# Optimization experiments

Measured on AMD Instinct MI355X. Metric: run time of the kernel, lower is better.

The kernel has to match this reference:

```python
import jax, jax.numpy as jnp
import numpy as np

EPS = 1e-5

def _ln(x):
    # non-affine LayerNorm over last dim
    m = jnp.mean(x, axis=-1, keepdims=True)
    v = jnp.var(x, axis=-1, keepdims=True)
    return (x - m) / jnp.sqrt(v + EPS)

def setup_inputs() -> dict:
    key = jax.random.key(0)
    ks = jax.random.split(key, 6)
    B, D_in, H = 16384, 512, 512
    bound_i = 1.0 / np.sqrt(D_in)
    bound_h = 1.0 / np.sqrt(H)
    x = jax.random.normal(ks[0], (B, D_in), dtype=jnp.float32)
    hx = jax.random.normal(ks[1], (B, H), dtype=jnp.float32)
    W_i2h = jax.random.uniform(ks[2], (3 * H, D_in), minval=-bound_i, maxval=bound_i, dtype=jnp.float32)
    b_i2h = jax.random.uniform(ks[3], (3 * H,), minval=-bound_i, maxval=bound_i, dtype=jnp.float32)
    W_h2h = jax.random.uniform(ks[4], (3 * H, H), minval=-bound_h, maxval=bound_h, dtype=jnp.float32)
    b_h2h = jax.random.uniform(ks[5], (3 * H,), minval=-bound_h, maxval=bound_h, dtype=jnp.float32)
    return {"x": x, "hx": hx, "W_i2h": W_i2h, "b_i2h": b_i2h, "W_h2h": W_h2h, "b_h2h": b_h2h}

def reference(x, hx, W_i2h, b_i2h, W_h2h, b_h2h):
    H = hx.shape[-1]
    xt = x @ W_i2h.T + b_i2h        # [B, 3H]
    ht = hx @ W_h2h.T + b_h2h       # [B, 3H]
    x_new = xt[:, 2 * H:]
    h_new = ht[:, 2 * H:]
    gates = jax.nn.sigmoid(_ln(xt[:, : 2 * H]) + _ln(ht[:, : 2 * H]))
    r_t = gates[:, :H]
    z_t = gates[:, H:]
    n_t = jnp.tanh(_ln(x_new) + r_t * _ln(h_new))
    h_t = z_t * hx + (1.0 - z_t) * n_t
    return h_t
```

## Files before the change

kernel.cpp:

```cpp
#include <hip/hip_runtime.h>

#define M_ROWS 16384
#define N_COLS 1536
#define K_DIM  512
#define H_DIM  512

typedef __attribute__((ext_vector_type(8))) short short8;
typedef __attribute__((ext_vector_type(16))) float f32x16;

__device__ __forceinline__ unsigned short f2bf(float f) {
  unsigned u = __float_as_uint(f);
  u += 0x7fffu + ((u >> 16) & 1u);
  return (unsigned short)(u >> 16);
}
__device__ __forceinline__ float bf2f(unsigned short h) {
  return __uint_as_float(((unsigned)h) << 16);
}

__device__ __forceinline__ void gload_lds16(const void* g, void* l) {
  __builtin_amdgcn_global_load_lds((const __attribute__((address_space(1))) void*)g,
                                   (__attribute__((address_space(3))) void*)l,
                                   16, 0, 0);
}

__global__ __launch_bounds__(256) void cvt_all(
    const float* __restrict__ x, const float* __restrict__ hx,
    const float* __restrict__ Wi, const float* __restrict__ Wh,
    unsigned short* __restrict__ xb, unsigned short* __restrict__ hxb,
    unsigned short* __restrict__ Wib, unsigned short* __restrict__ Whb) {
  int i = blockIdx.x * blockDim.x + threadIdx.x;
  const float* s; unsigned short* d; int off;
  if (i < 2097152)      { s = x;  d = xb;  off = i; }
  else if (i < 4194304) { s = hx; d = hxb; off = i - 2097152; }
  else if (i < 4390912) { s = Wi; d = Wib; off = i - 4194304; }
  else                  { s = Wh; d = Whb; off = i - 4390912; }
  float4 f = ((const float4*)s)[off];
  ushort4 u;
  u.x = f2bf(f.x); u.y = f2bf(f.y); u.z = f2bf(f.z); u.w = f2bf(f.w);
  ((ushort4*)d)[off] = u;
}

__global__ __launch_bounds__(256, 4) void gemm_bf16(
    const unsigned short* __restrict__ xb, const unsigned short* __restrict__ hxb,
    const unsigned short* __restrict__ Wib, const unsigned short* __restrict__ Whb,
    const float* __restrict__ b_i2h, const float* __restrict__ b_h2h,
    unsigned short* __restrict__ xt, unsigned short* __restrict__ ht) {
  const int mat = blockIdx.z;
  const unsigned short* A  = mat ? hxb : xb;
  const unsigned short* Bw = mat ? Whb : Wib;
  const float* bias        = mat ? b_h2h : b_i2h;
  unsigned short* outp     = mat ? ht : xt;

  const int m0 = blockIdx.x * 128;
  const int n0 = blockIdx.y * 128;

  __shared__ short lds[2 * 128 * 64];
  short* ldsA = lds;
  short* ldsB = lds + 128 * 64;

  const int t = threadIdx.x;
  const int w = t >> 6, lane = t & 63;
  const int w_row = w >> 1, w_col = w & 1;
  const int l31 = lane & 31, h = lane >> 5;

  f32x16 acc[2][2];
#pragma unroll
  for (int i = 0; i < 2; ++i)
#pragma unroll
    for (int j = 0; j < 2; ++j)
#pragma unroll
      for (int r = 0; r < 16; ++r) acc[i][j][r] = 0.f;

  const int srow = lane >> 3;
  const int scol = ((lane & 7) ^ srow) * 8;

  for (int k0 = 0; k0 < K_DIM; k0 += 64) {
#pragma unroll
    for (int q = 0; q < 4; ++q) {
      const int base_row = w * 32 + q * 8;
      gload_lds16(A  + (size_t)(m0 + base_row + srow) * K_DIM + k0 + scol,
                  &ldsA[base_row * 64]);
      gload_lds16(Bw + (size_t)(n0 + base_row + srow) * K_DIM + k0 + scol,
                  &ldsB[base_row * 64]);
    }
    __syncthreads();
#pragma unroll
    for (int kk = 0; kk < 4; ++kk) {
      const int chunk = ((kk * 2 + h) ^ (l31 & 7)) * 8;
      short8 af[2], bf[2];
#pragma unroll
      for (int i = 0; i < 2; ++i)
        af[i] = *(const short8*)&ldsA[(w_row * 64 + i * 32 + l31) * 64 + chunk];
#pragma unroll
      for (int j = 0; j < 2; ++j)
        bf[j] = *(const short8*)&ldsB[(w_col * 64 + j * 32 + l31) * 64 + chunk];
#pragma unroll
      for (int i = 0; i < 2; ++i)
#pragma unroll
        for (int j = 0; j < 2; ++j)
          acc[i][j] = __builtin_amdgcn_mfma_f32_32x32x16_bf16(af[i], bf[j], acc[i][j], 0, 0, 0);
    }
    __syncthreads();
  }

  float bj0[2], bj1[2];
#pragma unroll
  for (int j = 0; j < 2; ++j) {
    bj0[j] = bias[n0 + w_col * 64 + 0 * 32 + l31] * 0.f;
  }
  const float biasj0 = bias[n0 + w_col * 64 + l31];
  const float biasj1 = bias[n0 + w_col * 64 + 32 + l31];

#pragma unroll
  for (int i = 0; i < 2; ++i) {
#pragma unroll
    for (int g = 0; g < 4; ++g) {
#pragma unroll
      for (int d = 0; d < 4; ++d) {
        const int reg = g * 4 + d;
        const int row = d + 8 * g + 4 * h;
        ushort2 pk;
        pk.x = f2bf(acc[i][0][reg] + biasj0);
        pk.y = f2bf(acc[i][1][reg] + biasj1);
        *(ushort2*)(outp + (size_t)(m0 + w_row * 64 + i * 32 + row) * N_COLS +
                    n0 + w_col * 64 + 2 * l31) = pk;
      }
    }
  }
}

__global__ __launch_bounds__(256) void finalize_kernel(
    const unsigned short* __restrict__ xt, const unsigned short* __restrict__ ht,
    const unsigned short* __restrict__ hxb, float* __restrict__ out) {
  const int w = threadIdx.x >> 6, lane = threadIdx.x & 63;
  const int b = blockIdx.x * 4 + w;
  const size_t rb = (size_t)b * N_COLS;

  short8 sxr = *(const short8*)&xt[rb + 8 * lane];
  short8 sxz = *(const short8*)&xt[rb + 512 + 8 * lane];
  short8 sxn = *(const short8*)&xt[rb + 1024 + 8 * lane];
  short8 shr = *(const short8*)&ht[rb + 8 * lane];
  short8 shz = *(const short8*)&ht[rb + 512 + 8 * lane];
  short8 shn = *(const short8*)&ht[rb + 1024 + 8 * lane];

  float vxr[8], vxz[8], vxn[8], vhr[8], vhz[8], vhn[8];
#pragma unroll
  for (int k = 0; k < 8; ++k) {
    vxr[k] = bf2f((unsigned short)sxr[k]);
    vxz[k] = bf2f((unsigned short)sxz[k]);
    vxn[k] = bf2f((unsigned short)sxn[k]);
    vhr[k] = bf2f((unsigned short)shr[k]);
    vhz[k] = bf2f((unsigned short)shz[k]);
    vhn[k] = bf2f((unsigned short)shn[k]);
  }

  float pr[8] = {0.f, 0.f, 0.f, 0.f, 0.f, 0.f, 0.f, 0.f};
#pragma unroll
  for (int k = 0; k < 8; ++k) {
    pr[0] += vxr[k] + vxz[k];
    pr[1] += vxr[k] * vxr[k] + vxz[k] * vxz[k];
    pr[2] += vxn[k];
    pr[3] += vxn[k] * vxn[k];
    pr[4] += vhr[k] + vhz[k];
    pr[5] += vhr[k] * vhr[k] + vhz[k] * vhz[k];
    pr[6] += vhn[k];
    pr[7] += vhn[k] * vhn[k];
  }
#pragma unroll
  for (int msk = 1; msk < 64; msk <<= 1)
#pragma unroll
    for (int k = 0; k < 8; ++k) pr[k] += __shfl_xor(pr[k], msk);

  const float inv2H = 1.f / 1024.f, invH = 1.f / 512.f;
  const float mx0 = pr[0] * inv2H;
  const float ix0 = rsqrtf(pr[1] * inv2H - mx0 * mx0 + 1e-5f);
  const float mx1 = pr[2] * invH;
  const float ix1 = rsqrtf(pr[3] * invH - mx1 * mx1 + 1e-5f);
  const float mh0 = pr[4] * inv2H;
  const float ih0 = rsqrtf(pr[5] * inv2H - mh0 * mh0 + 1e-5f);
  const float mh1 = pr[6] * invH;
  const float ih1 = rsqrtf(pr[7] * invH - mh1 * mh1 + 1e-5f);

  auto calc = [&](float xrv, float xzv, float xnv, float hrv, float hzv,
                  float hnv, float hxs) -> float {
    float ar = (xrv - mx0) * ix0 + (hrv - mh0) * ih0;
    float az = (xzv - mx0) * ix0 + (hzv - mh0) * ih0;
    float r = 1.f / (1.f + __expf(-ar));
    float z = 1.f / (1.f + __expf(-az));
    float arg = (xnv - mx1) * ix1 + r * ((hnv - mh1) * ih1);
    float e2 = __expf(2.f * arg);
    float nn = (e2 - 1.f) / (e2 + 1.f);
    return z * hxs + (1.f - z) * nn;
  };

  const int base4 = 64 * (lane >> 3) + 4 * (lane & 7);
  const unsigned short* hxrow = hxb + (size_t)b * H_DIM;
  float* orow = out + (size_t)b * H_DIM;

  ushort4 hx0u = *(const ushort4*)&hxrow[base4];
  ushort4 hx1u = *(const ushort4*)&hxrow[base4 + 32];
  float hx0[4] = {bf2f(hx0u.x), bf2f(hx0u.y), bf2f(hx0u.z), bf2f(hx0u.w)};
  float hx1[4] = {bf2f(hx1u.x), bf2f(hx1u.y), bf2f(hx1u.z), bf2f(hx1u.w)};

  float4 r0, r1;
  float* r0p = (float*)&r0;
  float* r1p = (float*)&r1;
#pragma unroll
  for (int k = 0; k < 4; ++k) {
    r0p[k] = calc(vxr[2 * k], vxz[2 * k], vxn[2 * k],
                  vhr[2 * k], vhz[2 * k], vhn[2 * k], hx0[k]);
    r1p[k] = calc(vxr[2 * k + 1], vxz[2 * k + 1], vxn[2 * k + 1],
                  vhr[2 * k + 1], vhz[2 * k + 1], vhn[2 * k + 1], hx1[k]);
  }
  *(float4*)&orow[base4] = r0;
  *(float4*)&orow[base4 + 32] = r1;
}

extern "C" void kernel_launch(void* const* d_in, const int* in_sizes, int n_in,
                              void* d_out, int out_size, void* d_ws, size_t ws_size,
                              hipStream_t stream) {
  const float* x  = (const float*)d_in[0];
  const float* hx = (const float*)d_in[1];
  const float* Wi = (const float*)d_in[2];
  const float* bi = (const float*)d_in[3];
  const float* Wh = (const float*)d_in[4];
  const float* bh = (const float*)d_in[5];
  float* out = (float*)d_out;

  char* ws = (char*)d_ws;
  unsigned short* xb  = (unsigned short*)(ws);
  unsigned short* hxb = (unsigned short*)(ws + 16777216);
  unsigned short* Wib = (unsigned short*)(ws + 33554432);
  unsigned short* Whb = (unsigned short*)(ws + 35127296);
  unsigned short* xt  = (unsigned short*)(ws + 36700160);
  unsigned short* ht  = (unsigned short*)(ws + 87031808);

  cvt_all<<<17920, 256, 0, stream>>>(x, hx, Wi, Wh, xb, hxb, Wib, Whb);

  gemm_bf16<<<dim3(M_ROWS / 128, N_COLS / 128, 2), 256, 0, stream>>>(
      xb, hxb, Wib, Whb, bi, bh, xt, ht);

  finalize_kernel<<<M_ROWS / 4, 256, 0, stream>>>(xt, ht, hxb, out);
}
```

Baseline: 205.2 us.

## Enlarge GEMM tiles to 256x256 with double-buffered LDS prefetch and grid swizzle

```diff
diff --git a/kernel.cpp b/kernel.cpp
--- a/kernel.cpp
+++ b/kernel.cpp
@@ -4,6 +4,7 @@
 #define N_COLS 1536
 #define K_DIM  512
 #define H_DIM  512
+#define NT     8
 
 typedef __attribute__((ext_vector_type(8))) short short8;
 typedef __attribute__((ext_vector_type(16))) float f32x16;
@@ -40,7 +41,7 @@
   ((ushort4*)d)[off] = u;
 }
 
-__global__ __launch_bounds__(256, 4) void gemm_bf16(
+__global__ __launch_bounds__(512, 2) void gemm_bf16(
     const unsigned short* __restrict__ xb, const unsigned short* __restrict__ hxb,
     const unsigned short* __restrict__ Wib, const unsigned short* __restrict__ Whb,
     const float* __restrict__ b_i2h, const float* __restrict__ b_h2h,
@@ -51,68 +52,87 @@
   const float* bias        = mat ? b_h2h : b_i2h;
   unsigned short* outp     = mat ? ht : xt;
 
-  const int m0 = blockIdx.x * 128;
-  const int n0 = blockIdx.y * 128;
-
-  __shared__ short lds[2 * 128 * 64];
-  short* ldsA = lds;
-  short* ldsB = lds + 128 * 64;
+  const int l  = blockIdx.x + 64 * blockIdx.y;
+  const int wg = (l & 7) * 48 + (l >> 3);
+  const int mb = (wg / 6) * 256;
+  const int nb = (wg % 6) * 256;
+
+  __shared__ short lds[65536];
 
   const int t = threadIdx.x;
   const int w = t >> 6, lane = t & 63;
-  const int w_row = w >> 1, w_col = w & 1;
+  const int wr = w >> 2, wc = w & 3;
   const int l31 = lane & 31, h = lane >> 5;
-
-  f32x16 acc[2][2];
-#pragma unroll
-  for (int i = 0; i < 2; ++i)
-#pragma unroll
-    for (int j = 0; j < 2; ++j)
-#pragma unroll
-      for (int r = 0; r < 16; ++r) acc[i][j][r] = 0.f;
-
   const int srow = lane >> 3;
   const int scol = ((lane & 7) ^ srow) * 8;
 
-  for (int k0 = 0; k0 < K_DIM; k0 += 64) {
+  auto stage = [&](int kt) {
+    short* sA = lds + (kt & 1) * 16384;
+    short* sB = lds + 32768 + (kt & 1) * 16384;
+    const int k0 = kt * 64;
 #pragma unroll
     for (int q = 0; q < 4; ++q) {
-      const int base_row = w * 32 + q * 8;
-      gload_lds16(A  + (size_t)(m0 + base_row + srow) * K_DIM + k0 + scol,
-                  &ldsA[base_row * 64]);
-      gload_lds16(Bw + (size_t)(n0 + base_row + srow) * K_DIM + k0 + scol,
-                  &ldsB[base_row * 64]);
-    }
-    __syncthreads();
+      const int br = q * 64 + w * 8;
+      gload_lds16(A  + (size_t)(mb + br + srow) * K_DIM + k0 + scol, &sA[br * 64]);
+      gload_lds16(Bw + (size_t)(nb + br + srow) * K_DIM + k0 + scol, &sB[br * 64]);
+    }
+  };
+
+  stage(0);
+  stage(1);
+
+  f32x16 acc[4][2];
+#pragma unroll
+  for (int i = 0; i < 4; ++i)
+#pragma unroll
+    for (int j = 0; j < 2; ++j)
+#pragma unroll
+      for (int r = 0; r < 16; ++r) acc[i][j][r] = 0.f;
+
+  asm volatile("s_waitcnt vmcnt(8)" ::: "memory");
+  __builtin_amdgcn_s_barrier();
+  asm volatile("" ::: "memory");
+
+  for (int kt = 0; kt < NT; ++kt) {
+    const short* lA = lds + (kt & 1) * 16384;
+    const short* lB = lds + 32768 + (kt & 1) * 16384;
 #pragma unroll
     for (int kk = 0; kk < 4; ++kk) {
       const int chunk = ((kk * 2 + h) ^ (l31 & 7)) * 8;
-      short8 af[2], bf[2];
-#pragma unroll
-      for (int i = 0; i < 2; ++i)
-        af[i] = *(const short8*)&ldsA[(w_row * 64 + i * 32 + l31) * 64 + chunk];
+      short8 af[4], bfr[2];
+#pragma unroll
+      for (int i = 0; i < 4; ++i)
+        af[i] = *(const short8*)&lA[(wr * 128 + i * 32 + l31) * 64 + chunk];
 #pragma unroll
       for (int j = 0; j < 2; ++j)
-        bf[j] = *(const short8*)&ldsB[(w_col * 64 + j * 32 + l31) * 64 + chunk];
-#pragma unroll
-      for (int i = 0; i < 2; ++i)
+        bfr[j] = *(const short8*)&lB[(wc * 64 + j * 32 + l31) * 64 + chunk];
+      __builtin_amdgcn_s_setprio(1);
+#pragma unroll
+      for (int i = 0; i < 4; ++i)
 #pragma unroll
         for (int j = 0; j < 2; ++j)
-          acc[i][j] = __builtin_amdgcn_mfma_f32_32x32x16_bf16(af[i], bf[j], acc[i][j], 0, 0, 0);
-    }
-    __syncthreads();
-  }
-
-  float bj0[2], bj1[2];
-#pragma unroll
-  for (int j = 0; j < 2; ++j) {
-    bj0[j] = bias[n0 + w_col * 64 + 0 * 32 + l31] * 0.f;
-  }
-  const float biasj0 = bias[n0 + w_col * 64 + l31];
-  const float biasj1 = bias[n0 + w_col * 64 + 32 + l31];
-
-#pragma unroll
-  for (int i = 0; i < 2; ++i) {
+          acc[i][j] = __builtin_amdgcn_mfma_f32_32x32x16_bf16(af[i], bfr[j], acc[i][j], 0, 0, 0);
+      __builtin_amdgcn_s_setprio(0);
+    }
+    if (kt < NT - 1) {
+      asm volatile("" ::: "memory");
+      __builtin_amdgcn_s_barrier();
+      asm volatile("" ::: "memory");
+      if (kt < NT - 2) {
+        stage(kt + 2);
+        asm volatile("s_waitcnt vmcnt(8)" ::: "memory");
+      } else {
+        asm volatile("s_waitcnt vmcnt(0)" ::: "memory");
+      }
+      __builtin_amdgcn_s_barrier();
+      asm volatile("" ::: "memory");
+    }
+  }
+
+  const float biasj0 = bias[nb + wc * 64 + l31];
+  const float biasj1 = bias[nb + wc * 64 + 32 + l31];
+#pragma unroll
+  for (int i = 0; i < 4; ++i) {
 #pragma unroll
     for (int g = 0; g < 4; ++g) {
 #pragma unroll
@@ -122,8 +142,8 @@
         ushort2 pk;
         pk.x = f2bf(acc[i][0][reg] + biasj0);
         pk.y = f2bf(acc[i][1][reg] + biasj1);
-        *(ushort2*)(outp + (size_t)(m0 + w_row * 64 + i * 32 + row) * N_COLS +
-                    n0 + w_col * 64 + 2 * l31) = pk;
+        *(ushort2*)(outp + (size_t)(mb + wr * 128 + i * 32 + row) * N_COLS +
+                    nb + wc * 64 + 2 * l31) = pk;
       }
     }
   }
@@ -237,7 +257,7 @@
 
   cvt_all<<<17920, 256, 0, stream>>>(x, hx, Wi, Wh, xb, hxb, Wib, Whb);
 
-  gemm_bf16<<<dim3(M_ROWS / 128, N_COLS / 128, 2), 256, 0, stream>>>(
+  gemm_bf16<<<dim3(64, 6, 2), 512, 0, stream>>>(
       xb, hxb, Wib, Whb, bi, bh, xt, ht);
 
   finalize_kernel<<<M_ROWS / 4, 256, 0, stream>>>(xt, ht, hxb, out);
```

New measurement: 202.0 us. Within noise of the previous version (-1.6%).

## Fuse activation fp32-to-bf16 conversion into GEMM A-loads with double-buffered B

Applied to the files above, without the earlier changes.

```diff
diff --git a/kernel.cpp b/kernel.cpp
--- a/kernel.cpp
+++ b/kernel.cpp
@@ -4,6 +4,7 @@
 #define N_COLS 1536
 #define K_DIM  512
 #define H_DIM  512
+#define NT     8
 
 typedef __attribute__((ext_vector_type(8))) short short8;
 typedef __attribute__((ext_vector_type(16))) float f32x16;
@@ -16,6 +17,11 @@
 __device__ __forceinline__ float bf2f(unsigned short h) {
   return __uint_as_float(((unsigned)h) << 16);
 }
+__device__ __forceinline__ unsigned cvt_pk_bf16(float lo, float hi) {
+  unsigned r;
+  asm("v_cvt_pk_bf16_f32 %0, %1, %2" : "=v"(r) : "v"(lo), "v"(hi));
+  return r;
+}
 
 __device__ __forceinline__ void gload_lds16(const void* g, void* l) {
   __builtin_amdgcn_global_load_lds((const __attribute__((address_space(1))) void*)g,
@@ -23,30 +29,26 @@
                                    16, 0, 0);
 }
 
-__global__ __launch_bounds__(256) void cvt_all(
-    const float* __restrict__ x, const float* __restrict__ hx,
+__global__ __launch_bounds__(256) void cvt_w(
     const float* __restrict__ Wi, const float* __restrict__ Wh,
-    unsigned short* __restrict__ xb, unsigned short* __restrict__ hxb,
     unsigned short* __restrict__ Wib, unsigned short* __restrict__ Whb) {
   int i = blockIdx.x * blockDim.x + threadIdx.x;
   const float* s; unsigned short* d; int off;
-  if (i < 2097152)      { s = x;  d = xb;  off = i; }
-  else if (i < 4194304) { s = hx; d = hxb; off = i - 2097152; }
-  else if (i < 4390912) { s = Wi; d = Wib; off = i - 4194304; }
-  else                  { s = Wh; d = Whb; off = i - 4390912; }
+  if (i < 196608) { s = Wi; d = Wib; off = i; }
+  else            { s = Wh; d = Whb; off = i - 196608; }
   float4 f = ((const float4*)s)[off];
   ushort4 u;
   u.x = f2bf(f.x); u.y = f2bf(f.y); u.z = f2bf(f.z); u.w = f2bf(f.w);
   ((ushort4*)d)[off] = u;
 }
 
-__global__ __launch_bounds__(256, 4) void gemm_bf16(
-    const unsigned short* __restrict__ xb, const unsigned short* __restrict__ hxb,
+__global__ __launch_bounds__(256, 3) void gemm_bf16(
+    const float* __restrict__ x, const float* __restrict__ hx,
     const unsigned short* __restrict__ Wib, const unsigned short* __restrict__ Whb,
     const float* __restrict__ b_i2h, const float* __restrict__ b_h2h,
     unsigned short* __restrict__ xt, unsigned short* __restrict__ ht) {
   const int mat = blockIdx.z;
-  const unsigned short* A  = mat ? hxb : xb;
+  const float* A32         = mat ? hx : x;
   const unsigned short* Bw = mat ? Whb : Wib;
   const float* bias        = mat ? b_h2h : b_i2h;
   unsigned short* outp     = mat ? ht : xt;
@@ -54,7 +56,7 @@
   const int m0 = blockIdx.x * 128;
   const int n0 = blockIdx.y * 128;
 
-  __shared__ short lds[2 * 128 * 64];
+  __shared__ short lds[3 * 128 * 64];
   short* ldsA = lds;
   short* ldsB = lds + 128 * 64;
 
@@ -62,55 +64,90 @@
   const int w = t >> 6, lane = t & 63;
   const int w_row = w >> 1, w_col = w & 1;
   const int l31 = lane & 31, h = lane >> 5;
-
-  f32x16 acc[2][2];
-#pragma unroll
-  for (int i = 0; i < 2; ++i)
-#pragma unroll
-    for (int j = 0; j < 2; ++j)
-#pragma unroll
-      for (int r = 0; r < 16; ++r) acc[i][j][r] = 0.f;
-
   const int srow = lane >> 3;
   const int scol = ((lane & 7) ^ srow) * 8;
 
-  for (int k0 = 0; k0 < K_DIM; k0 += 64) {
+  const int arow_s = w * 32 + (lane >> 3);
+  const int ag = lane & 7;
+  float4 areg[8];
+  auto issueA = [&](int kt) {
+    const int k0 = kt * 64;
+#pragma unroll
+    for (int s = 0; s < 4; ++s) {
+      const float* src = A32 + (size_t)(m0 + arow_s + s * 8) * K_DIM + k0 + ag * 8;
+      areg[2 * s]     = *(const float4*)src;
+      areg[2 * s + 1] = *(const float4*)(src + 4);
+    }
+  };
+  auto issueB = [&](int kt) {
+    short* sB = ldsB + (kt & 1) * 8192;
+    const int k0 = kt * 64;
 #pragma unroll
     for (int q = 0; q < 4; ++q) {
-      const int base_row = w * 32 + q * 8;
-      gload_lds16(A  + (size_t)(m0 + base_row + srow) * K_DIM + k0 + scol,
-                  &ldsA[base_row * 64]);
-      gload_lds16(Bw + (size_t)(n0 + base_row + srow) * K_DIM + k0 + scol,
-                  &ldsB[base_row * 64]);
-    }
+      const int br = w * 32 + q * 8;
+      gload_lds16(Bw + (size_t)(n0 + br + srow) * K_DIM + k0 + scol, &sB[br * 64]);
+    }
+  };
+  auto writeA = [&]() {
+#pragma unroll
+    for (int s = 0; s < 4; ++s) {
+      const int r = arow_s + s * 8;
+      float4 f0 = areg[2 * s], f1 = areg[2 * s + 1];
+      uint4 u;
+      u.x = cvt_pk_bf16(f0.x, f0.y);
+      u.y = cvt_pk_bf16(f0.z, f0.w);
+      u.z = cvt_pk_bf16(f1.x, f1.y);
+      u.w = cvt_pk_bf16(f1.z, f1.w);
+      *(uint4*)&ldsA[r * 64 + ((ag ^ (r & 7)) * 8)] = u;
+    }
+  };
+
+  f32x16 acc[2][2];
+#pragma unroll
+  for (int i = 0; i < 2; ++i)
+#pragma unroll
+    for (int j = 0; j < 2; ++j)
+#pragma unroll
+      for (int r = 0; r < 16; ++r) acc[i][j][r] = 0.f;
+
+  issueA(0);
+  issueB(0);
+
+  for (int kt = 0; kt < NT; ++kt) {
+    writeA();
     __syncthreads();
+    if (kt < NT - 1) {
+      issueA(kt + 1);
+      issueB(kt + 1);
+    }
+    const short* lB = ldsB + (kt & 1) * 8192;
 #pragma unroll
     for (int kk = 0; kk < 4; ++kk) {
       const int chunk = ((kk * 2 + h) ^ (l31 & 7)) * 8;
-      short8 af[2], bf[2];
+      short8 af[2], bfr[2];
 #pragma unroll
       for (int i = 0; i < 2; ++i)
         af[i] = *(const short8*)&ldsA[(w_row * 64 + i * 32 + l31) * 64 + chunk];
 #pragma unroll
       for (int j = 0; j < 2; ++j)
-        bf[j] = *(const short8*)&ldsB[(w_col * 64 + j * 32 + l31) * 64 + chunk];
+        bfr[j] = *(const short8*)&lB[(w_col * 64 + j * 32 + l31) * 64 + chunk];
+      __builtin_amdgcn_s_setprio(1);
 #pragma unroll
       for (int i = 0; i < 2; ++i)
 #pragma unroll
         for (int j = 0; j < 2; ++j)
-          acc[i][j] = __builtin_amdgcn_mfma_f32_32x32x16_bf16(af[i], bf[j], acc[i][j], 0, 0, 0);
-    }
-    __syncthreads();
-  }
-
-  float bj0[2], bj1[2];
-#pragma unroll
-  for (int j = 0; j < 2; ++j) {
-    bj0[j] = bias[n0 + w_col * 64 + 0 * 32 + l31] * 0.f;
-  }
+          acc[i][j] = __builtin_amdgcn_mfma_f32_32x32x16_bf16(af[i], bfr[j], acc[i][j], 0, 0, 0);
+      __builtin_amdgcn_s_setprio(0);
+    }
+    if (kt < NT - 1) {
+      asm volatile("" ::: "memory");
+      __builtin_amdgcn_s_barrier();
+      asm volatile("" ::: "memory");
+    }
+  }
+
   const float biasj0 = bias[n0 + w_col * 64 + l31];
   const float biasj1 = bias[n0 + w_col * 64 + 32 + l31];
-
 #pragma unroll
   for (int i = 0; i < 2; ++i) {
 #pragma unroll
@@ -131,7 +168,7 @@
 
 __global__ __launch_bounds__(256) void finalize_kernel(
     const unsigned short* __restrict__ xt, const unsigned short* __restrict__ ht,
-    const unsigned short* __restrict__ hxb, float* __restrict__ out) {
+    const float* __restrict__ hx, float* __restrict__ out) {
   const int w = threadIdx.x >> 6, lane = threadIdx.x & 63;
   const int b = blockIdx.x * 4 + w;
   const size_t rb = (size_t)b * N_COLS;
@@ -194,13 +231,13 @@
   };
 
   const int base4 = 64 * (lane >> 3) + 4 * (lane & 7);
-  const unsigned short* hxrow = hxb + (size_t)b * H_DIM;
+  const float* hxrow = hx + (size_t)b * H_DIM;
   float* orow = out + (size_t)b * H_DIM;
 
-  ushort4 hx0u = *(const ushort4*)&hxrow[base4];
-  ushort4 hx1u = *(const ushort4*)&hxrow[base4 + 32];
-  float hx0[4] = {bf2f(hx0u.x), bf2f(hx0u.y), bf2f(hx0u.z), bf2f(hx0u.w)};
-  float hx1[4] = {bf2f(hx1u.x), bf2f(hx1u.y), bf2f(hx1u.z), bf2f(hx1u.w)};
+  float4 hx0 = *(const float4*)&hxrow[base4];
+  float4 hx1 = *(const float4*)&hxrow[base4 + 32];
+  const float* h0p = (const float*)&hx0;
+  const float* h1p = (const float*)&hx1;
 
   float4 r0, r1;
   float* r0p = (float*)&r0;
@@ -208,9 +245,9 @@
 #pragma unroll
   for (int k = 0; k < 4; ++k) {
     r0p[k] = calc(vxr[2 * k], vxz[2 * k], vxn[2 * k],
-                  vhr[2 * k], vhz[2 * k], vhn[2 * k], hx0[k]);
+                  vhr[2 * k], vhz[2 * k], vhn[2 * k], h0p[k]);
     r1p[k] = calc(vxr[2 * k + 1], vxz[2 * k + 1], vxn[2 * k + 1],
-                  vhr[2 * k + 1], vhz[2 * k + 1], vhn[2 * k + 1], hx1[k]);
+                  vhr[2 * k + 1], vhz[2 * k + 1], vhn[2 * k + 1], h1p[k]);
   }
   *(float4*)&orow[base4] = r0;
   *(float4*)&orow[base4 + 32] = r1;
@@ -228,17 +265,15 @@
   float* out = (float*)d_out;
 
   char* ws = (char*)d_ws;
-  unsigned short* xb  = (unsigned short*)(ws);
-  unsigned short* hxb = (unsigned short*)(ws + 16777216);
-  unsigned short* Wib = (unsigned short*)(ws + 33554432);
-  unsigned short* Whb = (unsigned short*)(ws + 35127296);
-  unsigned short* xt  = (unsigned short*)(ws + 36700160);
-  unsigned short* ht  = (unsigned short*)(ws + 87031808);
-
-  cvt_all<<<17920, 256, 0, stream>>>(x, hx, Wi, Wh, xb, hxb, Wib, Whb);
+  unsigned short* Wib = (unsigned short*)(ws);
+  unsigned short* Whb = (unsigned short*)(ws + 1572864);
+  unsigned short* xt  = (unsigned short*)(ws + 3145728);
+  unsigned short* ht  = (unsigned short*)(ws + 53477376);
+
+  cvt_w<<<1536, 256, 0, stream>>>(Wi, Wh, Wib, Whb);
 
   gemm_bf16<<<dim3(M_ROWS / 128, N_COLS / 128, 2), 256, 0, stream>>>(
-      xb, hxb, Wib, Whb, bi, bh, xt, ht);
-
-  finalize_kernel<<<M_ROWS / 4, 256, 0, stream>>>(xt, ht, hxb, out);
-}
+      x, hx, Wib, Whb, bi, bh, xt, ht);
+
+  finalize_kernel<<<M_ROWS / 4, 256, 0, stream>>>(xt, ht, hx, out);
+}
```

After: 205.9 us. About the same (+0.3%).
